# Optimization experiments

Measured on AMD Instinct MI355X. Metric: run time of the kernel, lower is better.

## Reference

```python
import jax, jax.numpy as jnp
import numpy as np

DIM = 512
CTX = 768
GROUPS = 32
EPS = 1e-5


def setup_inputs() -> dict:
    key = jax.random.key(0)
    ks = jax.random.split(key, 12)
    B, H, W, S = 16, 64, 64, 256
    x = jax.random.normal(ks[0], (B, DIM, H, W), dtype=jnp.float32)
    context = jax.random.normal(ks[1], (B, S, CTX), dtype=jnp.float32)
    gn_w = jnp.ones((DIM,), jnp.float32)
    gn_b = jnp.zeros((DIM,), jnp.float32)
    ln_w = jnp.ones((CTX,), jnp.float32)
    ln_b = jnp.zeros((CTX,), jnp.float32)
    wq = jax.random.normal(ks[2], (DIM, DIM), jnp.float32) * (DIM ** -0.5)
    bq = jnp.zeros((DIM,), jnp.float32)
    wkv = jax.random.normal(ks[3], (2 * DIM, CTX), jnp.float32) * (CTX ** -0.5)
    bkv = jnp.zeros((2 * DIM,), jnp.float32)
    wo = jax.random.normal(ks[4], (DIM, DIM), jnp.float32) * (DIM ** -0.5)
    bo = jnp.zeros((DIM,), jnp.float32)
    return {"x": x, "context": context, "gn_w": gn_w, "gn_b": gn_b,
            "ln_w": ln_w, "ln_b": ln_b, "wq": wq, "bq": bq,
            "wkv": wkv, "bkv": bkv, "wo": wo, "bo": bo}


def reference(x, context, gn_w, gn_b, ln_w, ln_b, wq, bq, wkv, bkv, wo, bo):
    b, c, h, w = x.shape
    scale = c ** -0.5
    # GroupNorm over (channels-per-group, H, W)
    xr = x.reshape(b, GROUPS, -1)
    mu = xr.mean(-1, keepdims=True)
    var = xr.var(-1, keepdims=True)
    xn = ((xr - mu) * jax.lax.rsqrt(var + EPS)).reshape(b, c, h, w)
    xn = xn * gn_w[None, :, None, None] + gn_b[None, :, None, None]
    # 1x1 conv query projection as channel GEMM
    q = jnp.einsum('bchw,oc->bohw', xn, wq) + bq[None, :, None, None]
    q = q.reshape(b, c, h * w).transpose(0, 2, 1)  # b, hw, c
    # LayerNorm on context
    cm = context.mean(-1, keepdims=True)
    cv = context.var(-1, keepdims=True)
    cn = (context - cm) * jax.lax.rsqrt(cv + EPS) * ln_w + ln_b
    kv = cn @ wkv.T + bkv  # b, s, 2c
    k, v = jnp.split(kv, 2, axis=-1)
    sim = jnp.einsum('bic,bjc->bij', q, k) * scale
    attn = jax.nn.softmax(sim, axis=-1)
    out = jnp.einsum('bij,bjc->bic', attn, v)
    out = out.transpose(0, 2, 1).reshape(b, c, h, w)
    out = jnp.einsum('bchw,oc->bohw', out, wo) + bo[None, :, None, None]
    return out + x
```

## Files before the change

### kernel.cpp

```cpp
#include <hip/hip_runtime.h>

typedef unsigned short u16;
typedef __attribute__((ext_vector_type(8))) short short8;
typedef __attribute__((ext_vector_type(4))) float f32x4;

#define DIM 512
#define CTX 768
#define HW 4096
#define NB 16
#define NS 256
#define EPSV 1e-5f

__device__ inline u16 f2bf(float f) {
    union { float f; unsigned u; } x; x.f = f;
    unsigned r = x.u + 0x7fffu + ((x.u >> 16) & 1u);
    return (u16)(r >> 16);
}
__device__ inline float bf2f(u16 v) {
    union { unsigned u; float f; } x; x.u = (unsigned)v << 16; return x.f;
}

__global__ void gn_stats(const float* __restrict__ x, const float* __restrict__ gn_w,
                         const float* __restrict__ gn_b, float* __restrict__ ga,
                         float* __restrict__ gd) {
    const int bg = blockIdx.x;
    const int b = bg >> 5, g = bg & 31;
    const float* base = x + ((long)b * DIM + g * 16) * HW;
    float s1 = 0.f, s2 = 0.f;
    const int tid = threadIdx.x;
    for (int i = tid; i < 16384; i += 256) {
        float4 v = ((const float4*)base)[i];
        s1 += v.x + v.y + v.z + v.w;
        s2 += v.x * v.x + v.y * v.y + v.z * v.z + v.w * v.w;
    }
    __shared__ float r1[256], r2[256];
    r1[tid] = s1; r2[tid] = s2; __syncthreads();
    for (int s = 128; s > 0; s >>= 1) {
        if (tid < s) { r1[tid] += r1[tid + s]; r2[tid] += r2[tid + s]; }
        __syncthreads();
    }
    __shared__ float mu_s, rs_s;
    if (tid == 0) {
        float mu = r1[0] * (1.f / 65536.f);
        float var = r2[0] * (1.f / 65536.f) - mu * mu;
        mu_s = mu; rs_s = rsqrtf(var + EPSV);
    }
    __syncthreads();
    if (tid < 16) {
        int c = g * 16 + tid;
        float aa = rs_s * gn_w[c];
        ga[b * DIM + c] = aa;
        gd[b * DIM + c] = gn_b[c] - mu_s * aa;
    }
}

__global__ void gn_apply_t(const float* __restrict__ x, const float* __restrict__ ga,
                           const float* __restrict__ gd, u16* __restrict__ xnt) {
    const int b = blockIdx.y;
    const int c0 = (blockIdx.x & 15) * 32;
    const int p0 = (blockIdx.x >> 4) * 32;
    const int tx = threadIdx.x & 31, ty = threadIdx.x >> 5;
    __shared__ u16 tile[32][33];
    #pragma unroll
    for (int i = 0; i < 4; i++) {
        int c = c0 + ty + i * 8;
        float v = x[((long)b * DIM + c) * HW + p0 + tx];
        v = v * ga[b * DIM + c] + gd[b * DIM + c];
        tile[ty + i * 8][tx] = f2bf(v);
    }
    __syncthreads();
    #pragma unroll
    for (int i = 0; i < 4; i++) {
        int p = p0 + ty + i * 8;
        xnt[((long)b * HW + p) * DIM + c0 + tx] = tile[tx][ty + i * 8];
    }
}

__global__ void ln_ctx(const float* __restrict__ ctx, const float* __restrict__ ln_w,
                       const float* __restrict__ ln_b, u16* __restrict__ cn) {
    const int row = blockIdx.x;
    const int tid = threadIdx.x;
    const float* r = ctx + (long)row * CTX;
    float v[3]; float s1 = 0.f, s2 = 0.f;
    #pragma unroll
    for (int i = 0; i < 3; i++) { v[i] = r[tid + i * 256]; s1 += v[i]; s2 += v[i] * v[i]; }
    __shared__ float r1[256], r2[256];
    r1[tid] = s1; r2[tid] = s2; __syncthreads();
    for (int s = 128; s > 0; s >>= 1) {
        if (tid < s) { r1[tid] += r1[tid + s]; r2[tid] += r2[tid + s]; }
        __syncthreads();
    }
    __shared__ float mu_s, rs_s;
    if (tid == 0) {
        float mu = r1[0] * (1.f / 768.f);
        float var = r2[0] * (1.f / 768.f) - mu * mu;
        mu_s = mu; rs_s = rsqrtf(var + EPSV);
    }
    __syncthreads();
    #pragma unroll
    for (int i = 0; i < 3; i++) {
        int idx = tid + i * 256;
        cn[(long)row * CTX + idx] = f2bf((v[i] - mu_s) * rs_s * ln_w[idx] + ln_b[idx]);
    }
}

__global__ void cvt_weights(const float* __restrict__ wq, const float* __restrict__ wkv,
                            const float* __restrict__ wo, u16* __restrict__ wqtb,
                            u16* __restrict__ wkvb, u16* __restrict__ wob) {
    int i = blockIdx.x * 256 + threadIdx.x;
    if (i < 262144) {
        wqtb[(i & 511) * 512 + (i >> 9)] = f2bf(wq[i]);
        wob[i] = f2bf(wo[i]);
    }
    if (i < 786432) wkvb[i] = f2bf(wkv[i]);
}

__global__ void kbias_k(const u16* __restrict__ k, const float* __restrict__ bq,
                        float* __restrict__ kbias) {
    const int row = blockIdx.x;
    const int tid = threadIdx.x;
    const u16* r = k + (long)row * DIM;
    float s = bf2f(r[tid]) * bq[tid] + bf2f(r[tid + 256]) * bq[tid + 256];
    __shared__ float red[256];
    red[tid] = s; __syncthreads();
    for (int st = 128; st > 0; st >>= 1) {
        if (tid < st) red[tid] += red[tid + st];
        __syncthreads();
    }
    if (tid == 0) kbias[row] = red[0];
}

template <int EPI>
__launch_bounds__(256, 2)
__global__ void gemm_nt(const u16* __restrict__ A, const u16* __restrict__ Bm,
                        const float* __restrict__ bias,
                        void* __restrict__ out0, void* __restrict__ out1,
                        int M, int N, int K, long batchA, long batchB,
                        long obatch, int ldo) {
    __shared__ u16 As[128][56];
    __shared__ u16 Bs[128][56];
    const int tid = threadIdx.x;
    const int lane = tid & 63;
    const int wave = tid >> 6;
    const int bb = blockIdx.y;
    const int tiles_n = N >> 7;
    const int m0 = (blockIdx.x / tiles_n) << 7;
    const int n0 = (blockIdx.x % tiles_n) << 7;
    const u16* Ab = A + (long)bb * batchA + (long)m0 * K;
    const u16* Bb = Bm + (long)bb * batchB + (long)n0 * K;

    const int sr = tid >> 2;
    const int sc = (tid & 3) << 3;
    const int l16 = lane & 15;
    const int quad = lane >> 4;
    const int wr = (wave >> 1) << 6;
    const int wc = (wave & 1) << 6;

    f32x4 acc[4][4] = {};

    for (int k0 = 0; k0 < K; k0 += 32) {
        __syncthreads();
        *(short8*)&As[sr][sc]      = *(const short8*)(Ab + (long)sr * K + k0 + sc);
        *(short8*)&As[sr + 64][sc] = *(const short8*)(Ab + (long)(sr + 64) * K + k0 + sc);
        *(short8*)&Bs[sr][sc]      = *(const short8*)(Bb + (long)sr * K + k0 + sc);
        *(short8*)&Bs[sr + 64][sc] = *(const short8*)(Bb + (long)(sr + 64) * K + k0 + sc);
        __syncthreads();
        short8 af[4], bfr[4];
        #pragma unroll
        for (int i = 0; i < 4; i++) af[i] = *(const short8*)&As[wr + i * 16 + l16][quad * 8];
        #pragma unroll
        for (int j = 0; j < 4; j++) bfr[j] = *(const short8*)&Bs[wc + j * 16 + l16][quad * 8];
        #pragma unroll
        for (int i = 0; i < 4; i++)
            #pragma unroll
            for (int j = 0; j < 4; j++)
                acc[i][j] = __builtin_amdgcn_mfma_f32_16x16x32_bf16(af[i], bfr[j], acc[i][j], 0, 0, 0);
    }

    #pragma unroll
    for (int i = 0; i < 4; i++) {
        #pragma unroll
        for (int r = 0; r < 4; r++) {
            const int row = m0 + wr + i * 16 + quad * 4 + r;
            #pragma unroll
            for (int j = 0; j < 4; j++) {
                const int col = n0 + wc + j * 16 + l16;
                float v = acc[i][j][r];
                if (EPI == 0) {
                    v += bias[col];
                    if (col < DIM) ((u16*)out0)[(long)bb * obatch + (long)row * ldo + col] = f2bf(v);
                    else           ((u16*)out1)[(long)bb * obatch + (long)row * ldo + (col - DIM)] = f2bf(v);
                } else if (EPI == 3) {
                    ((u16*)out0)[(long)bb * obatch + (long)row * ldo + col] = f2bf(v);
                } else {
                    ((u16*)out0)[(long)bb * obatch + (long)col * ldo + row] = f2bf(v);
                }
            }
        }
    }
}

__launch_bounds__(512, 2)
__global__ void flash_attn(const u16* __restrict__ xnt, const u16* __restrict__ Kq,
                           const u16* __restrict__ Vot, const float* __restrict__ kbias,
                           const float* __restrict__ bo, const float* __restrict__ x,
                           float* __restrict__ out) {
    __shared__ __align__(16) char fsm[153728];
    u16 (*P)[264]      = (u16(*)[264])(fsm);
    u16 (*As)[56]      = (u16(*)[56])(fsm + 67584);
    u16 (*Bs)[56]      = (u16(*)[56])(fsm + 67584 + 128 * 56 * 2);
    u16 (*Vs)[264]     = (u16(*)[264])(fsm + 67584);
    float (*red)[4]    = (float(*)[4])(fsm + 135168);
    float (*lbuf)[129] = (float(*)[129])(fsm + 137216);

    const int tid = threadIdx.x;
    const int lane = tid & 63;
    const int wave = tid >> 6;
    const int mw = wave >> 2;
    const int nw = wave & 3;
    const int l16 = lane & 15;
    const int quad = lane >> 4;
    const int b = blockIdx.y;
    const int m0 = blockIdx.x << 7;

    const u16* Ab = xnt + ((long)b * HW + m0) * DIM;
    const u16* Bb = Kq + (long)b * NS * DIM;

    f32x4 acc[4][4] = {};
    for (int k0 = 0; k0 < DIM; k0 += 32) {
        __syncthreads();
        {
            const int r = tid >> 2, c = (tid & 3) << 3;
            *(short8*)&As[r][c] = *(const short8*)(Ab + (long)r * DIM + k0 + c);
            const int r2 = tid >> 1, c2 = (tid & 1) << 4;
            *(short8*)&Bs[r2][c2]     = *(const short8*)(Bb + (long)r2 * DIM + k0 + c2);
            *(short8*)&Bs[r2][c2 + 8] = *(const short8*)(Bb + (long)r2 * DIM + k0 + c2 + 8);
        }
        __syncthreads();
        short8 af[4], bfr[4];
        #pragma unroll
        for (int i = 0; i < 4; i++) af[i] = *(const short8*)&As[mw * 64 + i * 16 + l16][quad * 8];
        #pragma unroll
        for (int j = 0; j < 4; j++) bfr[j] = *(const short8*)&Bs[nw * 64 + j * 16 + l16][quad * 8];
        #pragma unroll
        for (int i = 0; i < 4; i++)
            #pragma unroll
            for (int j = 0; j < 4; j++)
                acc[i][j] = __builtin_amdgcn_mfma_f32_16x16x32_bf16(af[i], bfr[j], acc[i][j], 0, 0, 0);
    }

    const float scale = 0.044194173824159216f;
    float kb[4];
    #pragma unroll
    for (int j = 0; j < 4; j++) kb[j] = kbias[b * NS + nw * 64 + j * 16 + l16];

    #pragma unroll
    for (int i = 0; i < 4; i++) {
        #pragma unroll
        for (int r = 0; r < 4; r++) {
            float m = -1e30f;
            #pragma unroll
            for (int j = 0; j < 4; j++) {
                float v = (acc[i][j][r] + kb[j]) * scale;
                acc[i][j][r] = v;
                m = fmaxf(m, v);
            }
            #pragma unroll
            for (int off = 1; off < 16; off <<= 1) m = fmaxf(m, __shfl_xor(m, off));
            if (l16 == 0) red[mw * 64 + i * 16 + quad * 4 + r][nw] = m;
        }
    }
    __syncthreads();
    float rsum[4][4];
    #pragma unroll
    for (int i = 0; i < 4; i++) {
        #pragma unroll
        for (int r = 0; r < 4; r++) {
            const int row = mw * 64 + i * 16 + quad * 4 + r;
            float4 rv = *(const float4*)red[row];
            float gm = fmaxf(fmaxf(rv.x, rv.y), fmaxf(rv.z, rv.w));
            float s = 0.f;
            #pragma unroll
            for (int j = 0; j < 4; j++) {
                float e = __expf(acc[i][j][r] - gm);
                acc[i][j][r] = e;
                s += e;
            }
            #pragma unroll
            for (int off = 1; off < 16; off <<= 1) s += __shfl_xor(s, off);
            rsum[i][r] = s;
        }
    }
    __syncthreads();
    #pragma unroll
    for (int i = 0; i < 4; i++)
        #pragma unroll
        for (int r = 0; r < 4; r++)
            if (l16 == 0) red[mw * 64 + i * 16 + quad * 4 + r][nw] = rsum[i][r];
    __syncthreads();
    #pragma unroll
    for (int i = 0; i < 4; i++) {
        #pragma unroll
        for (int r = 0; r < 4; r++) {
            const int row = mw * 64 + i * 16 + quad * 4 + r;
            float4 sv = *(const float4*)red[row];
            float inv = 1.f / (sv.x + sv.y + sv.z + sv.w);
            #pragma unroll
            for (int j = 0; j < 4; j++)
                P[row][nw * 64 + j * 16 + l16] = f2bf(acc[i][j][r] * inv);
        }
    }

    for (int nc = 0; nc < 4; nc++) {
        __syncthreads();
        {
            const u16* Vb = Vot + ((long)b * DIM + nc * 128) * NS;
            const int r = tid >> 2, c0 = (tid & 3) << 6;
            #pragma unroll
            for (int u = 0; u < 4; u++)
                *(short8*)&Vs[r][c0 + u * 8] = *(const short8*)(Vb + (long)r * NS + c0 + u * 8);
            #pragma unroll
            for (int u = 4; u < 8; u++)
                *(short8*)&Vs[r][c0 + u * 8] = *(const short8*)(Vb + (long)r * NS + c0 + u * 8);
        }
        __syncthreads();
        f32x4 oacc[4][2];
        #pragma unroll
        for (int i = 0; i < 4; i++)
            #pragma unroll
            for (int jj = 0; jj < 2; jj++)
                oacc[i][jj] = (f32x4){0.f, 0.f, 0.f, 0.f};
        #pragma unroll
        for (int kk = 0; kk < 8; kk++) {
            short8 pf[4], vf[2];
            #pragma unroll
            for (int i = 0; i < 4; i++)
                pf[i] = *(const short8*)&P[mw * 64 + i * 16 + l16][kk * 32 + quad * 8];
            #pragma unroll
            for (int jj = 0; jj < 2; jj++)
                vf[jj] = *(const short8*)&Vs[nw * 32 + jj * 16 + l16][kk * 32 + quad * 8];
            #pragma unroll
            for (int i = 0; i < 4; i++)
                #pragma unroll
                for (int jj = 0; jj < 2; jj++)
                    oacc[i][jj] = __builtin_amdgcn_mfma_f32_16x16x32_bf16(pf[i], vf[jj], oacc[i][jj], 0, 0, 0);
        }
        #pragma unroll
        for (int t = 0; t < 4; t++) {
            if (t > 0) __syncthreads();
            if (nw == t) {
                #pragma unroll
                for (int jj = 0; jj < 2; jj++)
                    #pragma unroll
                    for (int i = 0; i < 4; i++)
                        #pragma unroll
                        for (int r = 0; r < 4; r++)
                            lbuf[jj * 16 + l16][mw * 64 + i * 16 + quad * 4 + r] = oacc[i][jj][r];
            }
            __syncthreads();
            {
                const int cl = tid >> 4;
                const int p8 = (tid & 15) * 8;
                const int cg = nc * 128 + t * 32 + cl;
                const long idx = ((long)b * DIM + cg) * HW + m0 + p8;
                const float bv = bo[cg];
                float4 v0 = *(const float4*)&lbuf[cl][p8];
                float4 v1 = *(const float4*)&lbuf[cl][p8 + 4];
                float4 x0 = *(const float4*)&x[idx];
                float4 x1 = *(const float4*)&x[idx + 4];
                v0.x += x0.x + bv; v0.y += x0.y + bv; v0.z += x0.z + bv; v0.w += x0.w + bv;
                v1.x += x1.x + bv; v1.y += x1.y + bv; v1.z += x1.z + bv; v1.w += x1.w + bv;
                *(float4*)&out[idx] = v0;
                *(float4*)&out[idx + 4] = v1;
            }
        }
    }
}

extern "C" void kernel_launch(void* const* d_in, const int* in_sizes, int n_in,
                              void* d_out, int out_size, void* d_ws, size_t ws_size,
                              hipStream_t stream) {
    const float* x    = (const float*)d_in[0];
    const float* ctx  = (const float*)d_in[1];
    const float* gn_w = (const float*)d_in[2];
    const float* gn_b = (const float*)d_in[3];
    const float* ln_w = (const float*)d_in[4];
    const float* ln_b = (const float*)d_in[5];
    const float* wq   = (const float*)d_in[6];
    const float* bq   = (const float*)d_in[7];
    const float* wkv  = (const float*)d_in[8];
    const float* bkv  = (const float*)d_in[9];
    const float* wo   = (const float*)d_in[10];
    const float* bo   = (const float*)d_in[11];

    char* ws = (char*)d_ws;
    u16*   xnt  = (u16*)(ws + 0);
    u16*   cn   = (u16*)(ws + 67108864);
    u16*   kb_  = (u16*)(ws + 73400320);
    u16*   vb_  = (u16*)(ws + 77594624);
    u16*   Kq   = (u16*)(ws + 81788928);
    u16*   Vot  = (u16*)(ws + 85983232);
    u16*   wqtb = (u16*)(ws + 90177536);
    u16*   wkvb = (u16*)(ws + 90701824);
    u16*   wob  = (u16*)(ws + 92274688);
    float* ga   = (float*)(ws + 92798976);
    float* gd   = ga + NB * DIM;
    float* kbias = (float*)(ws + 92864512);

    gn_stats<<<dim3(NB * 32), dim3(256), 0, stream>>>(x, gn_w, gn_b, ga, gd);
    gn_apply_t<<<dim3(2048, NB), dim3(256), 0, stream>>>(x, ga, gd, xnt);
    ln_ctx<<<dim3(NB * NS), dim3(256), 0, stream>>>(ctx, ln_w, ln_b, cn);
    cvt_weights<<<dim3(3072), dim3(256), 0, stream>>>(wq, wkv, wo, wqtb, wkvb, wob);

    gemm_nt<0><<<dim3(2 * 8, NB), dim3(256), 0, stream>>>(
        cn, wkvb, bkv, kb_, vb_, NS, 2 * DIM, CTX,
        (long)NS * CTX, 0, (long)NS * DIM, DIM);
    gemm_nt<3><<<dim3(2 * 4, NB), dim3(256), 0, stream>>>(
        kb_, wqtb, nullptr, Kq, nullptr, NS, DIM, DIM,
        (long)NS * DIM, 0, (long)NS * DIM, DIM);
    kbias_k<<<dim3(NB * NS), dim3(256), 0, stream>>>(kb_, bq, kbias);
    gemm_nt<5><<<dim3(2 * 4, NB), dim3(256), 0, stream>>>(
        vb_, wob, nullptr, Vot, nullptr, NS, DIM, DIM,
        (long)NS * DIM, 0, (long)DIM * NS, NS);
    flash_attn<<<dim3(32, NB), dim3(512), 0, stream>>>(
        xnt, Kq, Vot, kbias, bo, x, (float*)d_out);
}
```

Baseline: 469.6 us.

## Shrink flash_attn shared memory, read V from global, vectorize GN transpose

The GroupNorm apply/transpose kernel now works on 64x64 tiles with float4 loads and 16-byte bf16 stores, launching fewer blocks with wider memory transactions. The flash attention kernel no longer stages V in shared memory; each wave reads its V fragments straight from global memory, and the LDS buffers are overlapped and cut to about half. This allows a launch bound of 4 blocks per CU, aiming for higher occupancy. The output epilogue now writes 16 channels per step over 8 steps. That adds more barriers and exposes uncached global V loads inside the MFMA loop, which may cost latency.

```diff
diff --git a/kernel.cpp b/kernel.cpp
--- a/kernel.cpp
+++ b/kernel.cpp
@@ -57,22 +57,34 @@
 __global__ void gn_apply_t(const float* __restrict__ x, const float* __restrict__ ga,
                            const float* __restrict__ gd, u16* __restrict__ xnt) {
     const int b = blockIdx.y;
-    const int c0 = (blockIdx.x & 15) * 32;
-    const int p0 = (blockIdx.x >> 4) * 32;
-    const int tx = threadIdx.x & 31, ty = threadIdx.x >> 5;
-    __shared__ u16 tile[32][33];
+    const int c0 = (blockIdx.x & 7) * 64;
+    const int p0 = (blockIdx.x >> 3) * 64;
+    __shared__ u16 t[64][68];
+    const int tid = threadIdx.x;
+    const int tc = tid >> 4;
+    const int tp = (tid & 15) * 4;
     #pragma unroll
     for (int i = 0; i < 4; i++) {
-        int c = c0 + ty + i * 8;
-        float v = x[((long)b * DIM + c) * HW + p0 + tx];
-        v = v * ga[b * DIM + c] + gd[b * DIM + c];
-        tile[ty + i * 8][tx] = f2bf(v);
-    }
-    __syncthreads();
-    #pragma unroll
-    for (int i = 0; i < 4; i++) {
-        int p = p0 + ty + i * 8;
-        xnt[((long)b * HW + p) * DIM + c0 + tx] = tile[tx][ty + i * 8];
+        const int c = c0 + tc + i * 16;
+        const float a = ga[b * DIM + c];
+        const float d = gd[b * DIM + c];
+        float4 v = *(const float4*)&x[((long)b * DIM + c) * HW + p0 + tp];
+        u16* dst = &t[tc + i * 16][tp];
+        dst[0] = f2bf(v.x * a + d);
+        dst[1] = f2bf(v.y * a + d);
+        dst[2] = f2bf(v.z * a + d);
+        dst[3] = f2bf(v.w * a + d);
+    }
+    __syncthreads();
+    const int wp = tid >> 3;
+    const int wc = (tid & 7) * 8;
+    #pragma unroll
+    for (int i = 0; i < 2; i++) {
+        const int p = wp + i * 32;
+        short8 o;
+        #pragma unroll
+        for (int k = 0; k < 8; k++) o[k] = t[wc + k][p];
+        *(short8*)&xnt[((long)b * HW + p0 + p) * DIM + c0 + wc] = o;
     }
 }
 
@@ -200,18 +212,17 @@
     }
 }
 
-__launch_bounds__(512, 2)
+__launch_bounds__(512, 4)
 __global__ void flash_attn(const u16* __restrict__ xnt, const u16* __restrict__ Kq,
                            const u16* __restrict__ Vot, const float* __restrict__ kbias,
                            const float* __restrict__ bo, const float* __restrict__ x,
                            float* __restrict__ out) {
-    __shared__ __align__(16) char fsm[153728];
+    __shared__ __align__(16) char fsm[78080];
+    u16 (*As)[56]      = (u16(*)[56])(fsm);
+    u16 (*Bs)[56]      = (u16(*)[56])(fsm + 14336);
     u16 (*P)[264]      = (u16(*)[264])(fsm);
-    u16 (*As)[56]      = (u16(*)[56])(fsm + 67584);
-    u16 (*Bs)[56]      = (u16(*)[56])(fsm + 67584 + 128 * 56 * 2);
-    u16 (*Vs)[264]     = (u16(*)[264])(fsm + 67584);
-    float (*red)[4]    = (float(*)[4])(fsm + 135168);
-    float (*lbuf)[129] = (float(*)[129])(fsm + 137216);
+    float (*red)[4]    = (float(*)[4])(fsm + 67584);
+    float (*lbuf)[132] = (float(*)[132])(fsm + 69632);
 
     const int tid = threadIdx.x;
     const int lane = tid & 63;
@@ -310,20 +321,10 @@
                 P[row][nw * 64 + j * 16 + l16] = f2bf(acc[i][j][r] * inv);
         }
     }
-
+    __syncthreads();
+
+    const u16* Vb = Vot + ((long)b * DIM + nw * 32 + l16) * NS + quad * 8;
     for (int nc = 0; nc < 4; nc++) {
-        __syncthreads();
-        {
-            const u16* Vb = Vot + ((long)b * DIM + nc * 128) * NS;
-            const int r = tid >> 2, c0 = (tid & 3) << 6;
-            #pragma unroll
-            for (int u = 0; u < 4; u++)
-                *(short8*)&Vs[r][c0 + u * 8] = *(const short8*)(Vb + (long)r * NS + c0 + u * 8);
-            #pragma unroll
-            for (int u = 4; u < 8; u++)
-                *(short8*)&Vs[r][c0 + u * 8] = *(const short8*)(Vb + (long)r * NS + c0 + u * 8);
-        }
-        __syncthreads();
         f32x4 oacc[4][2];
         #pragma unroll
         for (int i = 0; i < 4; i++)
@@ -338,7 +339,7 @@
                 pf[i] = *(const short8*)&P[mw * 64 + i * 16 + l16][kk * 32 + quad * 8];
             #pragma unroll
             for (int jj = 0; jj < 2; jj++)
-                vf[jj] = *(const short8*)&Vs[nw * 32 + jj * 16 + l16][kk * 32 + quad * 8];
+                vf[jj] = *(const short8*)(Vb + (long)(nc * 128 + jj * 16) * NS + kk * 32);
             #pragma unroll
             for (int i = 0; i < 4; i++)
                 #pragma unroll
@@ -346,32 +347,27 @@
                     oacc[i][jj] = __builtin_amdgcn_mfma_f32_16x16x32_bf16(pf[i], vf[jj], oacc[i][jj], 0, 0, 0);
         }
         #pragma unroll
-        for (int t = 0; t < 4; t++) {
-            if (t > 0) __syncthreads();
-            if (nw == t) {
+        for (int t = 0; t < 8; t++) {
+            __syncthreads();
+            if (nw == (t >> 1)) {
+                const int jj = t & 1;
                 #pragma unroll
-                for (int jj = 0; jj < 2; jj++)
+                for (int i = 0; i < 4; i++)
                     #pragma unroll
-                    for (int i = 0; i < 4; i++)
-                        #pragma unroll
-                        for (int r = 0; r < 4; r++)
-                            lbuf[jj * 16 + l16][mw * 64 + i * 16 + quad * 4 + r] = oacc[i][jj][r];
+                    for (int r = 0; r < 4; r++)
+                        lbuf[l16][mw * 64 + i * 16 + quad * 4 + r] = oacc[i][jj][r];
             }
             __syncthreads();
             {
-                const int cl = tid >> 4;
-                const int p8 = (tid & 15) * 8;
-                const int cg = nc * 128 + t * 32 + cl;
-                const long idx = ((long)b * DIM + cg) * HW + m0 + p8;
+                const int cl = tid >> 5;
+                const int p4 = (tid & 31) * 4;
+                const int cg = nc * 128 + t * 16 + cl;
+                const long idx = ((long)b * DIM + cg) * HW + m0 + p4;
                 const float bv = bo[cg];
-                float4 v0 = *(const float4*)&lbuf[cl][p8];
-                float4 v1 = *(const float4*)&lbuf[cl][p8 + 4];
+                float4 v0 = *(const float4*)&lbuf[cl][p4];
                 float4 x0 = *(const float4*)&x[idx];
-                float4 x1 = *(const float4*)&x[idx + 4];
                 v0.x += x0.x + bv; v0.y += x0.y + bv; v0.z += x0.z + bv; v0.w += x0.w + bv;
-                v1.x += x1.x + bv; v1.y += x1.y + bv; v1.z += x1.z + bv; v1.w += x1.w + bv;
                 *(float4*)&out[idx] = v0;
-                *(float4*)&out[idx + 4] = v1;
             }
         }
     }
@@ -408,7 +404,7 @@
     float* kbias = (float*)(ws + 92864512);
 
     gn_stats<<<dim3(NB * 32), dim3(256), 0, stream>>>(x, gn_w, gn_b, ga, gd);
-    gn_apply_t<<<dim3(2048, NB), dim3(256), 0, stream>>>(x, ga, gd, xnt);
+    gn_apply_t<<<dim3(512, NB), dim3(256), 0, stream>>>(x, ga, gd, xnt);
     ln_ctx<<<dim3(NB * NS), dim3(256), 0, stream>>>(ctx, ln_w, ln_b, cn);
     cvt_weights<<<dim3(3072), dim3(256), 0, stream>>>(wq, wkv, wo, wqtb, wkvb, wob);
 
```

After: 441.9 us. 5.9% less time.
